# Optimization experiments

Measured on AMD Instinct MI355X. Metric: run time of the kernel, lower is better.

## Reference

```python
import jax, jax.numpy as jnp
import numpy as np

B, C, T, H, W, TS = 4, 512, 2048, 8, 16, 1000
D = C // H  # head_dim = 64
SCALE = D ** -0.5


def _conv1x1(w, b, z):
    # torch Conv1d(dim, dim, 1): (B,C,T) -> (B,C,T)
    return jnp.einsum('oc,bct->bot', w, z) + b[None, :, None]


def _linear(w, b, z):
    # torch Linear: z @ w.T + b, w is (out,in)
    return z @ w.T + b


def _rope(x, cos, sin):
    # x: (B,H,T,D); cos/sin: (T, D//2) broadcast over (B,H)
    x1, x2 = x[..., ::2], x[..., 1::2]
    r = jnp.stack([x1 * cos - x2 * sin, x1 * sin + x2 * cos], axis=-1)
    return r.reshape(x.shape)


def _local(x, cond, qw, qb, kw, kb, vw, vb, ow, ob):
    q = _conv1x1(qw, qb, x)
    k = _conv1x1(kw, kb, cond)
    v = _conv1x1(vw, vb, cond)
    pl = W // 2
    pr = W - pl - 1
    kp = jnp.pad(k, ((0, 0), (0, 0), (pl, pr)))
    vp = jnp.pad(v, ((0, 0), (0, 0), (pl, pr)))
    idx = jnp.arange(T)[:, None] + jnp.arange(W)[None, :]  # (T,W)
    ku = kp[:, :, idx].reshape(B, H, D, T, W)
    vu = vp[:, :, idx].reshape(B, H, D, T, W)
    qh = q.reshape(B, H, D, T)
    dots = jnp.einsum('bhdt,bhdtw->bhtw', qh, ku) * SCALE
    attn = jax.nn.softmax(dots, axis=-1)
    out = jnp.einsum('bhtw,bhdtw->bhdt', attn, vu)
    # faithful to torch: permute(0,1,3,2).contiguous().view(B,C,T)
    out = out.transpose(0, 1, 3, 2).reshape(B, C, T)
    return _conv1x1(ow, ob, out)


def _global(xg, cg, qw, qb, kw, kb, vw, vb, ow, ob):
    # xg, cg: (B,T,C)
    q = _linear(qw, qb, xg).reshape(B, T, H, D).transpose(0, 2, 1, 3)
    k = _linear(kw, kb, cg).reshape(B, T, H, D).transpose(0, 2, 1, 3)
    v = _linear(vw, vb, cg).reshape(B, T, H, D).transpose(0, 2, 1, 3)
    inv_freq = 1.0 / (10000.0 ** (jnp.arange(0, D, 2, dtype=jnp.float32) / D))
    pos = jnp.arange(T, dtype=jnp.float32)
    sinus = pos[:, None] * inv_freq[None, :]  # (T, D//2)
    cos, sin = jnp.cos(sinus), jnp.sin(sinus)
    q = _rope(q, cos, sin)
    k = _rope(k, cos, sin)
    dots = jnp.einsum('bhqd,bhkd->bhqk', q, k) * SCALE
    attn = jax.nn.softmax(dots, axis=-1)
    out = jnp.einsum('bhqk,bhkd->bhqd', attn, v)
    out = out.transpose(0, 2, 1, 3).reshape(B, T, C)
    return _linear(ow, ob, out)


def setup_inputs() -> dict:
    key = jax.random.key(0)
    ks = jax.random.split(key, 20)
    pm = lambda k: jax.random.normal(k, (C, C), dtype=jnp.float32) * 0.02
    pb = lambda k: jax.random.normal(k, (C,), dtype=jnp.float32) * 0.02
    return {
        'x': jax.random.normal(ks[0], (B, C, T), dtype=jnp.float32),
        'cond': jax.random.normal(ks[1], (B, C, T), dtype=jnp.float32),
        't': jax.random.randint(ks[2], (B,), 0, TS),
        'lq_w': pm(ks[3]), 'lq_b': pb(ks[4]),
        'lk_w': pm(ks[5]), 'lk_b': pb(ks[6]),
        'lv_w': pm(ks[7]), 'lv_b': pb(ks[8]),
        'lo_w': pm(ks[9]), 'lo_b': pb(ks[10]),
        'gq_w': pm(ks[11]), 'gq_b': pb(ks[12]),
        'gk_w': pm(ks[13]), 'gk_b': pb(ks[14]),
        'gv_w': pm(ks[15]), 'gv_b': pb(ks[16]),
        'go_w': pm(ks[17]), 'go_b': pb(ks[18]),
    }


def reference(x, cond, t, lq_w, lq_b, lk_w, lk_b, lv_w, lv_b, lo_w, lo_b,
              gq_w, gq_b, gk_w, gk_b, gv_w, gv_b, go_w, go_b):
    ctx_local = _local(x, cond, lq_w, lq_b, lk_w, lk_b, lv_w, lv_b, lo_w, lo_b)
    ctx_global = _global(x.transpose(0, 2, 1), cond.transpose(0, 2, 1),
                         gq_w, gq_b, gk_w, gk_b, gv_w, gv_b, go_w, go_b)
    ctx_global = ctx_global.transpose(0, 2, 1)  # (B,C,T)
    t_norm = t.astype(jnp.float32) / jnp.float32(TS - 1)
    a_g = (1.0 - t_norm)[:, None, None]
    a_l = t_norm[:, None, None]
    return jnp.sqrt(a_g) * ctx_global + jnp.sqrt(a_l) * ctx_local
```

## Files before the change

kernel.cpp:

```cpp
#include <hip/hip_runtime.h>
#include <math.h>

#define BB 4
#define CC 512
#define TT 2048
#define HH 8
#define DD 64

static constexpr float SCALE = 0.125f;
static constexpr float QK_SCALE_LOG2 = 0.125f * 1.4426950408889634f;

typedef __attribute__((ext_vector_type(8)))  short  short8;
typedef __attribute__((ext_vector_type(4)))  float  f32x4;
typedef __attribute__((ext_vector_type(16))) float  f32x16;
typedef __attribute__((ext_vector_type(2)))  unsigned int u32x2;

static __device__ __forceinline__ ushort f2bf(float f) {
    uint u = __float_as_uint(f);
    uint r = (u + 0x7fffu + ((u >> 16) & 1u)) >> 16;
    return (ushort)r;
}
static __device__ __forceinline__ float bf2f(ushort u) {
    return __uint_as_float((uint)u << 16);
}

typedef unsigned int u32;
typedef u32 __attribute__((address_space(1))) gu32;
typedef u32 __attribute__((address_space(3))) lu32;
static __device__ __forceinline__ void gload_lds16(const void* g, void* l) {
    __builtin_amdgcn_global_load_lds((const gu32*)g, (lu32*)l, 16, 0, 0);
}

__global__ __launch_bounds__(256)
void prep_kernel(const float* __restrict__ x, const float* __restrict__ cond,
                 const float* w0, const float* w1, const float* w2, const float* w3,
                 const float* w4, const float* w5, const float* w6, const float* w7,
                 ushort* __restrict__ wbf, ushort* __restrict__ wc,
                 ushort* __restrict__ xtb, ushort* __restrict__ ctb,
                 float* __restrict__ ctab, float* __restrict__ stab)
{
    __shared__ ushort L[64][66];
    int bid = blockIdx.x;
    const int tid = threadIdx.x;

    if (bid < 256) {
        int idx = bid * 256 + tid;
        int i = idx >> 11;
        int t = idx & 2047;
        float ex   = (2.0f * (float)i) / 64.0f;
        float invf = powf(10000.0f, -ex);
        float ang  = (float)t * invf;
        ctab[idx] = cosf(ang);
        stab[idx] = sinf(ang);
        return;
    }
    bid -= 256;
    if (bid < 2048) {
        const float* srcs[8] = {w0, w1, w2, w3, w4, w5, w6, w7};
        int wi = bid >> 8;
        int idx = ((bid & 255) * 256 + tid) * 4;
        float4 v = *(const float4*)&srcs[wi][idx];
        uint lo = (uint)f2bf(v.x) | ((uint)f2bf(v.y) << 16);
        uint hi = (uint)f2bf(v.z) | ((uint)f2bf(v.w) << 16);
        uint2 pk = make_uint2(lo, hi);
        if (wi < 6) {
            *(uint2*)&wbf[(size_t)wi * 262144 + idx] = pk;
        } else {
            int row = idx >> 9, col = idx & 511;
            *(uint2*)&wc[(size_t)row * 1024 + (wi - 6) * 512 + col] = pk;
        }
        return;
    }
    bid -= 2048;
    const int z = bid >> 8;
    const int r = bid & 255;
    const float* in = (z < 4) ? x : cond;
    ushort* outp    = (z < 4) ? xtb : ctb;
    const int b = z & 3;
    const int t0 = (r & 31) * 64, c0 = (r >> 5) * 64;
    const float* inb = in + (size_t)b * CC * TT;
    ushort* outb = outp + (size_t)b * TT * CC;
    const int lc = tid >> 6;
    const int lt = tid & 63;
    #pragma unroll
    for (int i = 0; i < 16; i++) {
        int c = i * 4 + lc;
        L[c][lt] = f2bf(inb[(size_t)(c0 + c) * TT + t0 + lt]);
    }
    __syncthreads();
    #pragma unroll
    for (int i = 0; i < 16; i++) {
        int t = i * 4 + lc;
        outb[(size_t)(t0 + t) * CC + c0 + lt] = L[lt][t];
    }
}

__global__ __launch_bounds__(256)
void transpose_bf16_kernel(const ushort* __restrict__ in, ushort* __restrict__ AG)
{
    __shared__ ushort L[64][66];
    const int t0 = blockIdx.x * 64, c0 = blockIdx.y * 64, b = blockIdx.z;
    const ushort* inb = in + (size_t)b * CC * TT;
    ushort* outb = AG + (size_t)b * TT * 1024;
    const int lc = threadIdx.x >> 6;
    const int lt = threadIdx.x & 63;
    #pragma unroll
    for (int i = 0; i < 16; i++) {
        int c = i * 4 + lc;
        L[c][lt] = inb[(size_t)(c0 + c) * TT + t0 + lt];
    }
    __syncthreads();
    #pragma unroll
    for (int i = 0; i < 16; i++) {
        int t = i * 4 + lc;
        outb[(size_t)(t0 + t) * 1024 + c0 + lt] = L[lt][t];
    }
}

#define GEMM_BODY(Wp, XTp, KD, NB)                                                  \
    __shared__ __align__(16) ushort As[2][128][32];                                 \
    __shared__ __align__(16) ushort Bs[2][NB][32];                                  \
    const int tid  = threadIdx.x;                                                   \
    const int wid  = tid >> 6;                                                      \
    const int lane = tid & 63;                                                      \
    const int x  = lane & 15;                                                       \
    const int gq = lane >> 4;                                                       \
    const int wm = wid >> 1, wn = wid & 1;                                          \
    const int m0 = blockIdx.y * 128;                                                \
    const int n0 = blockIdx.x * NB;                                                 \
    const int srow = lane >> 2;                                                     \
    const int sblk = lane & 3;                                                      \
    f32x4 acc[4][NB / 32];                                                          \
    _Pragma("unroll")                                                               \
    for (int i = 0; i < 4; i++)                                                     \
        _Pragma("unroll")                                                           \
        for (int j = 0; j < NB / 32; j++) acc[i][j] = (f32x4){0.f, 0.f, 0.f, 0.f};  \
    auto stage = [&](int bf, int k0) {                                              \
        _Pragma("unroll")                                                           \
        for (int c = 0; c < 2; c++) {                                               \
            int row = c * 64 + wid * 16 + srow;                                     \
            int dbk = sblk ^ ((row >> 1) & 3);                                      \
            gload_lds16(&Wp[(size_t)(m0 + row) * KD + k0 + dbk * 8],                \
                        &As[bf][c * 64 + wid * 16][0]);                             \
            if (c * 64 < NB)                                                        \
                gload_lds16(&XTp[(size_t)(n0 + row) * KD + k0 + dbk * 8],           \
                            &Bs[bf][c * 64 + wid * 16][0]);                         \
        }                                                                           \
    };                                                                              \
    stage(0, 0);                                                                    \
    __syncthreads();                                                                \
    for (int ks = 0; ks < (KD) / 32; ks++) {                                        \
        int cur = ks & 1;                                                           \
        if (ks < (KD) / 32 - 1) stage(cur ^ 1, (ks + 1) * 32);                      \
        short8 aF[4], bF[NB / 32];                                                  \
        _Pragma("unroll")                                                           \
        for (int mi = 0; mi < 4; mi++) {                                            \
            int row = wm * 64 + mi * 16 + x;                                        \
            aF[mi] = *(const short8*)&As[cur][row][(gq ^ ((row >> 1) & 3)) * 8];    \
        }                                                                           \
        _Pragma("unroll")                                                           \
        for (int nj = 0; nj < NB / 32; nj++) {                                      \
            int row = wn * (NB / 2) + nj * 16 + x;                                  \
            bF[nj] = *(const short8*)&Bs[cur][row][(gq ^ ((row >> 1) & 3)) * 8];    \
        }                                                                           \
        _Pragma("unroll")                                                           \
        for (int mi = 0; mi < 4; mi++)                                              \
            _Pragma("unroll")                                                       \
            for (int nj = 0; nj < NB / 32; nj++)                                    \
                acc[mi][nj] = __builtin_amdgcn_mfma_f32_16x16x32_bf16(aF[mi], bF[nj], acc[mi][nj], 0, 0, 0); \
        __syncthreads();                                                            \
    }

__global__ __launch_bounds__(512, 4)
void gemm6_kernel(const ushort* __restrict__ wbase,
                  const float* __restrict__ b0, const float* __restrict__ b1, const float* __restrict__ b2,
                  const float* __restrict__ b3, const float* __restrict__ b4, const float* __restrict__ b5,
                  const ushort* __restrict__ xtb, const ushort* __restrict__ ctb,
                  ushort* __restrict__ y0, ushort* __restrict__ y1, ushort* __restrict__ y2,
                  ushort* __restrict__ y3, ushort* __restrict__ y4, ushort* __restrict__ y5,
                  const float* __restrict__ ctab, const float* __restrict__ stab)
{
    __shared__ __align__(16) ushort SMEM[16384];
    ushort (*As)[128][32] = (ushort(*)[128][32])&SMEM[0];
    ushort (*Bs)[128][32] = (ushort(*)[128][32])&SMEM[8192];

    const int z = blockIdx.z;
    const ushort* Wp  = wbase + (size_t)z * 262144;
    const float* bias = (z == 0) ? b0 : (z == 1) ? b1 : (z == 2) ? b2 : (z == 3) ? b3 : (z == 4) ? b4 : b5;
    const ushort* XTp = (z == 0 || z == 3) ? xtb : ctb;
    ushort* Y = (z == 0) ? y0 : (z == 1) ? y1 : (z == 2) ? y2 : (z == 3) ? y3 : (z == 4) ? y4 : y5;
    const bool do_rope = (z == 3 || z == 4);
    const bool swp = (z == 5);
    const float qscale = (z == 3) ? QK_SCALE_LOG2 : 1.0f;

    const int tid  = threadIdx.x;
    const int wid  = tid >> 6;
    const int lane = tid & 63;
    const int x  = lane & 15;
    const int gq = lane >> 4;
    const int wm = wid >> 2;
    const int wn = wid & 3;
    const int m0 = blockIdx.y * 128;
    const int n0 = blockIdx.x * 128;
    const int srow = lane >> 2;
    const int sblk = lane & 3;

    f32x4 acc[4][2];
    #pragma unroll
    for (int i = 0; i < 4; i++)
        #pragma unroll
        for (int j = 0; j < 2; j++) acc[i][j] = (f32x4){0.f, 0.f, 0.f, 0.f};

    auto stage = [&](int bf, int k0) {
        int row = wid * 16 + srow;
        int dbk = sblk ^ ((row >> 1) & 3);
        gload_lds16(&Wp[(size_t)(m0 + row) * 512 + k0 + dbk * 8],
                    &As[bf][wid * 16][0]);
        gload_lds16(&XTp[(size_t)(n0 + row) * 512 + k0 + dbk * 8],
                    &Bs[bf][wid * 16][0]);
    };
    stage(0, 0);
    __syncthreads();

    for (int ks = 0; ks < 16; ks++) {
        int cur = ks & 1;
        if (ks < 15) stage(cur ^ 1, (ks + 1) * 32);
        short8 aF[4], bF[2];
        #pragma unroll
        for (int mi = 0; mi < 4; mi++) {
            int row = wm * 64 + mi * 16 + x;
            aF[mi] = *(const short8*)&As[cur][row][(gq ^ ((row >> 1) & 3)) * 8];
        }
        #pragma unroll
        for (int nj = 0; nj < 2; nj++) {
            int row = wn * 32 + nj * 16 + x;
            bF[nj] = *(const short8*)&Bs[cur][row][(gq ^ ((row >> 1) & 3)) * 8];
        }
        if (swp) {
            #pragma unroll
            for (int mi = 0; mi < 4; mi++)
                #pragma unroll
                for (int nj = 0; nj < 2; nj++)
                    acc[mi][nj] = __builtin_amdgcn_mfma_f32_16x16x32_bf16(bF[nj], aF[mi], acc[mi][nj], 0, 0, 0);
        } else {
            #pragma unroll
            for (int mi = 0; mi < 4; mi++)
                #pragma unroll
                for (int nj = 0; nj < 2; nj++)
                    acc[mi][nj] = __builtin_amdgcn_mfma_f32_16x16x32_bf16(aF[mi], bF[nj], acc[mi][nj], 0, 0, 0);
        }
        __syncthreads();
    }

    if (!swp) {
        #pragma unroll
        for (int mi = 0; mi < 4; mi++) {
            const int cL = wm * 64 + mi * 16 + 4 * gq;
            const int mb = m0 + cL;
            float bv[4];
            #pragma unroll
            for (int r = 0; r < 4; r++) bv[r] = bias[mb + r];
            #pragma unroll
            for (int nj = 0; nj < 2; nj++) {
                const int tL = wn * 32 + nj * 16 + x;
                const int tt = (n0 + tL) & 2047;
                f32x4 v = acc[mi][nj];
                v[0] += bv[0]; v[1] += bv[1]; v[2] += bv[2]; v[3] += bv[3];
                if (do_rope) {
                    const int i0 = (mb & 63) >> 1;
                    float c0 = ctab[(size_t)i0 * 2048 + tt],       s0 = stab[(size_t)i0 * 2048 + tt];
                    float c1 = ctab[(size_t)(i0 + 1) * 2048 + tt], s1 = stab[(size_t)(i0 + 1) * 2048 + tt];
                    float e0 = (v[0] * c0 - v[1] * s0) * qscale;
                    float e1 = (v[0] * s0 + v[1] * c0) * qscale;
                    float e2 = (v[2] * c1 - v[3] * s1) * qscale;
                    float e3 = (v[2] * s1 + v[3] * c1) * qscale;
                    v[0] = e0; v[1] = e1; v[2] = e2; v[3] = e3;
                }
                uint lo = (uint)f2bf(v[0]) | ((uint)f2bf(v[1]) << 16);
                uint hi = (uint)f2bf(v[2]) | ((uint)f2bf(v[3]) << 16);
                const int blk = (cL >> 3) ^ (tL & 7);
                *(uint2*)&SMEM[tL * 128 + blk * 8 + (gq & 1) * 4] = make_uint2(lo, hi);
            }
        }
    } else {
        #pragma unroll
        for (int mi = 0; mi < 4; mi++) {
            const int cL = wm * 64 + mi * 16 + x;
            const float bv = bias[m0 + cL];
            #pragma unroll
            for (int nj = 0; nj < 2; nj++) {
                const int tL = wn * 32 + nj * 16 + 4 * gq;
                f32x4 v = acc[mi][nj];
                uint lo = (uint)f2bf(v[0] + bv) | ((uint)f2bf(v[1] + bv) << 16);
                uint hi = (uint)f2bf(v[2] + bv) | ((uint)f2bf(v[3] + bv) << 16);
                const int blk = (tL >> 3) ^ (cL & 7);
                *(uint2*)&SMEM[cL * 128 + blk * 8 + (gq & 1) * 4] = make_uint2(lo, hi);
            }
        }
    }
    __syncthreads();

    if (z <= 3) {
        #pragma unroll
        for (int s = 0; s < 4; s++) {
            const int chunk = s * 512 + tid;
            const int row = chunk >> 4;
            const int blk = chunk & 15;
            uint4 val = *(const uint4*)&SMEM[row * 128 + ((blk ^ (row & 7)) << 3)];
            *(uint4*)&Y[(size_t)(n0 + row) * 512 + m0 + blk * 8] = val;
        }
    } else if (z == 4) {
        const int bidx = n0 >> 11;
        #pragma unroll
        for (int s = 0; s < 4; s++) {
            const int chunk = s * 512 + tid;
            const int row = chunk & 127;
            const int blk = chunk >> 7;
            uint4 val = *(const uint4*)&SMEM[row * 128 + ((blk ^ (row & 7)) << 3)];
            const int tt = (n0 + row) & 2047;
            const int kt = tt >> 6, tk = tt & 63, sb = tk >> 5, qh = tk & 31;
            const int c = m0 + blk * 8;
            const int hh = (c >> 6) & 7, d = c & 63;
            const int kap = d >> 4, hb = (d >> 3) & 1;
            size_t off = (size_t)(bidx * 8 + hh) * 131072
                       + (size_t)(((((kt * 2 + sb) * 4 + kap) * 2 + hb) * 32 + qh) * 8);
            *(uint4*)&Y[off] = val;
        }
    } else {
        const int bidx = n0 >> 11;
        #pragma unroll
        for (int s = 0; s < 4; s++) {
            const int chunk = s * 512 + tid;
            const int rowc = chunk & 127;
            const int blk = chunk >> 7;
            uint4 val = *(const uint4*)&SMEM[rowc * 128 + ((blk ^ (rowc & 7)) << 3)];
            const int c = m0 + rowc;
            const int hh = (c >> 6) & 7, d = c & 63;
            const int qh = d & 31, db = (d >> 5) & 1;
            const int tt0 = (n0 + blk * 8) & 2047;
            const int kt = tt0 >> 6, kk = tt0 & 63;
            const int kc = kk >> 4, hb = (kk >> 3) & 1;
            size_t off = (size_t)(bidx * 8 + hh) * 131072
                       + (size_t)(((((kt * 2 + db) * 4 + kc) * 2 + hb) * 32 + qh) * 8);
            *(uint4*)&Y[off] = val;
        }
    }
}

__global__ __launch_bounds__(256)
void gemm_comb_kernel(const ushort* __restrict__ Wp,
                      const float* __restrict__ bl, const float* __restrict__ bg,
                      const ushort* __restrict__ XTp, float* __restrict__ Y,
                      const int* __restrict__ tarr)
{
    GEMM_BODY(Wp, XTp, 1024, 64)

    const int bidx = (n0 + wn * 32) >> 11;
    float tn = (float)tarr[bidx] / 999.0f;
    float sl = sqrtf(tn), sg = sqrtf(1.0f - tn);

    #pragma unroll
    for (int mi = 0; mi < 4; mi++) {
        const int mb = m0 + wm * 64 + mi * 16 + 4 * gq;
        float bv[4];
        #pragma unroll
        for (int r = 0; r < 4; r++) bv[r] = sl * bl[mb + r] + sg * bg[mb + r];
        #pragma unroll
        for (int nj = 0; nj < 2; nj++) {
            const int tt = (n0 + wn * 32 + nj * 16 + x) & 2047;
            f32x4 v = acc[mi][nj];
            #pragma unroll
            for (int r = 0; r < 4; r++)
                Y[((size_t)bidx * 512 + mb + r) * 2048 + tt] = v[r] + bv[r];
        }
    }
}

__global__ __launch_bounds__(256)
void local_attn_kernel(const ushort* __restrict__ qt, const ushort* __restrict__ kt,
                       const ushort* __restrict__ vt, ushort* __restrict__ outb,
                       const int* __restrict__ tarr)
{
    const int gidx = blockIdx.x * 256 + threadIdx.x;
    const int lane = threadIdx.x & 63;
    const int qu = lane >> 4;
    const int wv = gidx >> 6;
    const int lin = wv * 16 + (lane & 15);
    const int t = lin & (TT - 1);
    const int h = (lin >> 11) & (HH - 1);
    const int b = lin >> 14;
    const size_t rb = (size_t)b * TT;
    const int co = h * DD + qu * 16;
    const float wl = sqrtf((float)tarr[b] / 999.0f);

    float qf[16];
    {
        const ushort* qp = qt + (rb + t) * 512 + co;
        #pragma unroll
        for (int i = 0; i < 2; i++) {
            short8 v = *(const short8*)&qp[i * 8];
            #pragma unroll
            for (int j = 0; j < 8; j++) qf[i * 8 + j] = bf2f((ushort)v[j]);
        }
    }

    int koff[16]; float msk[16];
    #pragma unroll
    for (int w = 0; w < 16; w++) {
        int kidx = t + w - 8;
        msk[w]  = (kidx >= 0 && kidx < TT) ? 1.0f : 0.0f;
        koff[w] = min(max(kidx, 0), TT - 1);
    }

    float dots[16];
    #pragma unroll
    for (int w = 0; w < 16; w++) {
        const ushort* kp = kt + (rb + koff[w]) * 512 + co;
        float d0 = 0.f, d1 = 0.f;
        #pragma unroll
        for (int i = 0; i < 2; i++) {
            short8 v = *(const short8*)&kp[i * 8];
            #pragma unroll
            for (int j = 0; j < 8; j += 2) {
                d0 = fmaf(qf[i * 8 + j],     bf2f((ushort)v[j]),     d0);
                d1 = fmaf(qf[i * 8 + j + 1], bf2f((ushort)v[j + 1]), d1);
            }
        }
        dots[w] = d0 + d1;
    }
    #pragma unroll
    for (int w = 0; w < 16; w++) {
        dots[w] += __shfl_xor(dots[w], 16);
        dots[w] += __shfl_xor(dots[w], 32);
    }

    float m = -1e30f;
    #pragma unroll
    for (int w = 0; w < 16; w++) { dots[w] = dots[w] * SCALE * msk[w]; m = fmaxf(m, dots[w]); }
    float p[16], s = 0.f;
    #pragma unroll
    for (int w = 0; w < 16; w++) { p[w] = __expf(dots[w] - m); s += p[w]; }
    float inv = wl / s;
    #pragma unroll
    for (int w = 0; w < 16; w++) p[w] *= msk[w] * inv;

    float oa[16];
    #pragma unroll
    for (int d = 0; d < 16; d++) oa[d] = 0.f;
    #pragma unroll
    for (int w = 0; w < 16; w++) {
        const ushort* vp = vt + (rb + koff[w]) * 512 + co;
        #pragma unroll
        for (int i = 0; i < 2; i++) {
            short8 v = *(const short8*)&vp[i * 8];
            #pragma unroll
            for (int j = 0; j < 8; j++)
                oa[i * 8 + j] = fmaf(p[w], bf2f((ushort)v[j]), oa[i * 8 + j]);
        }
    }

    ushort* op = outb + ((size_t)b * CC + h * DD + (t >> 5)) * TT + (size_t)(t & 31) * DD + qu * 16;
    #pragma unroll
    for (int i = 0; i < 2; i++) {
        uint w0 = (uint)f2bf(oa[i * 8 + 0]) | ((uint)f2bf(oa[i * 8 + 1]) << 16);
        uint w1 = (uint)f2bf(oa[i * 8 + 2]) | ((uint)f2bf(oa[i * 8 + 3]) << 16);
        uint w2 = (uint)f2bf(oa[i * 8 + 4]) | ((uint)f2bf(oa[i * 8 + 5]) << 16);
        uint w3 = (uint)f2bf(oa[i * 8 + 6]) | ((uint)f2bf(oa[i * 8 + 7]) << 16);
        *(uint4*)&op[i * 8] = make_uint4(w0, w1, w2, w3);
    }
}

__global__ __launch_bounds__(512)
void flash_global_kernel(const ushort* __restrict__ qtd, const ushort* __restrict__ KT,
                         const ushort* __restrict__ VT, ushort* __restrict__ AG,
                         const int* __restrict__ tarr)
{
    __shared__ __align__(16) ushort Ks[2][2][4096];
    __shared__ __align__(16) ushort Vs[2][2][4096];

    const int tid  = threadIdx.x;
    const int grp  = tid >> 8;
    const int t8   = tid & 255;
    const int w    = t8 >> 6;
    const int lane = tid & 63;
    const int qh   = lane & 31;
    const int h    = lane >> 5;

    const int bid = blockIdx.x;
    const int sw  = (bid & 7) * 64 + (bid >> 3);
    const int qt  = sw & 15;
    const int p   = sw >> 4;
    const int hh  = p & 7, b = p >> 3;

    const size_t kvbase = (size_t)p * 131072 + (size_t)grp * (16 * 4096);
    const size_t btd    = (size_t)b * TT;
    const int q_glob = qt * 128 + w * 32 + qh;
    const float sg_mix = sqrtf(1.0f - (float)tarr[b] / 999.0f);

    short8 aQ[4];
    {
        const ushort* qrow = qtd + (btd + q_glob) * 512 + hh * 64;
        #pragma unroll
        for (int kap = 0; kap < 4; kap++)
            aQ[kap] = *(const short8*)&qrow[kap * 16 + h * 8];
    }

    f32x16 oacc[2];
    #pragma unroll
    for (int d = 0; d < 2; d++)
        #pragma unroll
        for (int r = 0; r < 16; r++) oacc[d][r] = 0.f;
    float l_run = 0.0f;

    const ushort* kA = KT + kvbase + (size_t)(2 * w) * 512 + lane * 8;
    const ushort* vA = VT + kvbase + (size_t)(2 * w) * 512 + lane * 8;

    auto issue = [&](int buf, int kt) {
        const size_t off = (size_t)kt * 4096;
        gload_lds16(kA + off,       &Ks[grp][buf][(2 * w) * 512]);
        gload_lds16(kA + off + 512, &Ks[grp][buf][(2 * w + 1) * 512]);
        gload_lds16(vA + off,       &Vs[grp][buf][(2 * w) * 512]);
        gload_lds16(vA + off + 512, &Vs[grp][buf][(2 * w + 1) * 512]);
    };
    issue(0, 0);

    int cur = 0;
    for (int kt = 0; kt < 16; kt++) {
        __syncthreads();
        if (kt < 15) issue(cur ^ 1, kt + 1);

        const ushort* KsC = &Ks[grp][cur][0];
        const ushort* VsC = &Vs[grp][cur][0];

        f32x16 ST[2];
        #pragma unroll
        for (int sb = 0; sb < 2; sb++)
            #pragma unroll
            for (int r = 0; r < 16; r++) ST[sb][r] = 0.f;
        __builtin_amdgcn_s_setprio(1);
        #pragma unroll
        for (int sb = 0; sb < 2; sb++)
            #pragma unroll
            for (int kap = 0; kap < 4; kap++) {
                short8 aK = *(const short8*)&KsC[(sb * 4 + kap) * 512 + lane * 8];
                ST[sb] = __builtin_amdgcn_mfma_f32_32x32x16_bf16(aK, aQ[kap], ST[sb], 0, 0, 0);
            }
        __builtin_amdgcn_s_setprio(0);

        float s0 = 0.f, s1 = 0.f, s2 = 0.f, s3 = 0.f;
        #pragma unroll
        for (int sb = 0; sb < 2; sb++)
            #pragma unroll
            for (int r = 0; r < 16; r += 4) {
                ST[sb][r + 0] = __builtin_amdgcn_exp2f(ST[sb][r + 0]);
                ST[sb][r + 1] = __builtin_amdgcn_exp2f(ST[sb][r + 1]);
                ST[sb][r + 2] = __builtin_amdgcn_exp2f(ST[sb][r + 2]);
                ST[sb][r + 3] = __builtin_amdgcn_exp2f(ST[sb][r + 3]);
                s0 += ST[sb][r + 0]; s1 += ST[sb][r + 1];
                s2 += ST[sb][r + 2]; s3 += ST[sb][r + 3];
            }
        l_run += (s0 + s1) + (s2 + s3);

        short8 bP[4];
        #pragma unroll
        for (int sb = 0; sb < 2; sb++)
            #pragma unroll
            for (int kcp = 0; kcp < 2; kcp++) {
                const int rb2 = kcp * 8;
                uint ca, cb, cc, cd;
                asm("v_cvt_pk_bf16_f32 %0, %1, %2" : "=v"(ca) : "v"(ST[sb][rb2 + 0]), "v"(ST[sb][rb2 + 1]));
                asm("v_cvt_pk_bf16_f32 %0, %1, %2" : "=v"(cb) : "v"(ST[sb][rb2 + 2]), "v"(ST[sb][rb2 + 3]));
                asm("v_cvt_pk_bf16_f32 %0, %1, %2" : "=v"(cc) : "v"(ST[sb][rb2 + 4]), "v"(ST[sb][rb2 + 5]));
                asm("v_cvt_pk_bf16_f32 %0, %1, %2" : "=v"(cd) : "v"(ST[sb][rb2 + 6]), "v"(ST[sb][rb2 + 7]));
                u32x2 r1 = __builtin_amdgcn_permlane32_swap(ca, cc, false, false);
                u32x2 r2 = __builtin_amdgcn_permlane32_swap(cb, cd, false, false);
                uint4 bu = make_uint4(r1[0], r2[0], r1[1], r2[1]);
                bP[sb * 2 + kcp] = __builtin_bit_cast(short8, bu);
            }

        __builtin_amdgcn_s_setprio(1);
        #pragma unroll
        for (int db = 0; db < 2; db++)
            #pragma unroll
            for (int kc = 0; kc < 4; kc++) {
                short8 aV = *(const short8*)&VsC[(db * 4 + kc) * 512 + lane * 8];
                oacc[db] = __builtin_amdgcn_mfma_f32_32x32x16_bf16(aV, bP[kc], oacc[db], 0, 0, 0);
            }
        __builtin_amdgcn_s_setprio(0);
        cur ^= 1;
    }

    __syncthreads();
    f32x4* OP = (f32x4*)&Ks[0][0][0];
    float* LP = (float*)&Vs[0][0][0];
    if (grp == 1) {
        #pragma unroll
        for (int j = 0; j < 8; j++)
            OP[j * 256 + t8] = (f32x4){oacc[j >> 2][(j & 3) * 4 + 0], oacc[j >> 2][(j & 3) * 4 + 1],
                                       oacc[j >> 2][(j & 3) * 4 + 2], oacc[j >> 2][(j & 3) * 4 + 3]};
        LP[t8] = l_run;
    }
    __syncthreads();
    if (grp == 0) {
        #pragma unroll
        for (int j = 0; j < 8; j++) {
            f32x4 o = OP[j * 256 + t8];
            oacc[j >> 2][(j & 3) * 4 + 0] += o[0];
            oacc[j >> 2][(j & 3) * 4 + 1] += o[1];
            oacc[j >> 2][(j & 3) * 4 + 2] += o[2];
            oacc[j >> 2][(j & 3) * 4 + 3] += o[3];
        }
        l_run += LP[t8];
        float ltot = l_run + __shfl_xor(l_run, 32);
        float inv = sg_mix / ltot;
        ushort* agrow = AG + (btd + q_glob) * 1024 + 512 + hh * 64;
        #pragma unroll
        for (int db = 0; db < 2; db++)
            #pragma unroll
            for (int rq = 0; rq < 4; rq++) {
                const int d0 = db * 32 + rq * 8 + h * 4;
                uint lo = (uint)f2bf(oacc[db][rq * 4 + 0] * inv) | ((uint)f2bf(oacc[db][rq * 4 + 1] * inv) << 16);
                uint hi = (uint)f2bf(oacc[db][rq * 4 + 2] * inv) | ((uint)f2bf(oacc[db][rq * 4 + 3] * inv) << 16);
                *(uint2*)&agrow[d0] = make_uint2(lo, hi);
            }
    }
}

extern "C" void kernel_launch(void* const* d_in, const int* in_sizes, int n_in,
                              void* d_out, int out_size, void* d_ws, size_t ws_size,
                              hipStream_t stream)
{
    const float* x    = (const float*)d_in[0];
    const float* cond = (const float*)d_in[1];
    const int*   tarr = (const int*)d_in[2];
    const float* lq_w = (const float*)d_in[3];
    const float* lq_b = (const float*)d_in[4];
    const float* lk_w = (const float*)d_in[5];
    const float* lk_b = (const float*)d_in[6];
    const float* lv_w = (const float*)d_in[7];
    const float* lv_b = (const float*)d_in[8];
    const float* lo_w = (const float*)d_in[9];
    const float* lo_b = (const float*)d_in[10];
    const float* gq_w = (const float*)d_in[11];
    const float* gq_b = (const float*)d_in[12];
    const float* gk_w = (const float*)d_in[13];
    const float* gk_b = (const float*)d_in[14];
    const float* gv_w = (const float*)d_in[15];
    const float* gv_b = (const float*)d_in[16];
    const float* go_w = (const float*)d_in[17];
    const float* go_b = (const float*)d_in[18];
    float* out = (float*)d_out;

    const size_t N = (size_t)BB * CC * TT;
    char* w = (char*)d_ws;
    ushort* xtb = (ushort*)w; w += N * 2;
    ushort* ctb = (ushort*)w; w += N * 2;
    ushort* lq  = (ushort*)w; w += N * 2;
    ushort* lk  = (ushort*)w; w += N * 2;
    ushort* lv  = (ushort*)w; w += N * 2;
    ushort* gqb = (ushort*)w; w += N * 2;
    ushort* ktb = (ushort*)w; w += N * 2;
    ushort* vtb = (ushort*)w; w += N * 2;
    ushort* scr = (ushort*)w; w += N * 2;
    ushort* AG  = (ushort*)w; w += (size_t)BB * TT * 1024 * 2;
    ushort* wbf = (ushort*)w; w += (size_t)6 * 512 * 512 * 2;
    ushort* wc  = (ushort*)w; w += (size_t)512 * 1024 * 2;
    float* ctab = (float*)w;  w += (size_t)32 * 2048 * 4;
    float* stab = (float*)w;

    dim3 blk(256);

    prep_kernel<<<dim3(4352), blk, 0, stream>>>(x, cond,
                                                lq_w, lk_w, lv_w, gq_w, gk_w, gv_w, lo_w, go_w,
                                                wbf, wc, xtb, ctb, ctab, stab);

    gemm6_kernel<<<dim3(64, 4, 6), dim3(512), 0, stream>>>(wbf, lq_b, lk_b, lv_b, gq_b, gk_b, gv_b,
                                                           xtb, ctb, lq, lk, lv, gqb, ktb, vtb, ctab, stab);

    local_attn_kernel<<<dim3(BB * HH * TT * 4 / 256), blk, 0, stream>>>(lq, lk, lv, scr, tarr);
    transpose_bf16_kernel<<<dim3(32, 8, BB), blk, 0, stream>>>(scr, AG);

    flash_global_kernel<<<dim3(512), dim3(512), 0, stream>>>(gqb, ktb, vtb, AG, tarr);

    gemm_comb_kernel<<<dim3(128, 4), blk, 0, stream>>>(wc, lo_b, go_b, AG, out, tarr);
}
```

Measured before the change: 154.9 us.

## Fuse local and global attention into one interleaved-block kernel launch

```diff
diff --git a/kernel.cpp b/kernel.cpp
--- a/kernel.cpp
+++ b/kernel.cpp
@@ -376,253 +376,255 @@
     }
 }
 
-__global__ __launch_bounds__(256)
-void local_attn_kernel(const ushort* __restrict__ qt, const ushort* __restrict__ kt,
+__global__ __launch_bounds__(512)
+void fused_attn_kernel(const ushort* __restrict__ qtd, const ushort* __restrict__ KT,
+                       const ushort* __restrict__ VT, ushort* __restrict__ AG,
+                       const ushort* __restrict__ qt, const ushort* __restrict__ kt,
                        const ushort* __restrict__ vt, ushort* __restrict__ outb,
                        const int* __restrict__ tarr)
 {
-    const int gidx = blockIdx.x * 256 + threadIdx.x;
-    const int lane = threadIdx.x & 63;
-    const int qu = lane >> 4;
-    const int wv = gidx >> 6;
-    const int lin = wv * 16 + (lane & 15);
-    const int t = lin & (TT - 1);
-    const int h = (lin >> 11) & (HH - 1);
-    const int b = lin >> 14;
-    const size_t rb = (size_t)b * TT;
-    const int co = h * DD + qu * 16;
-    const float wl = sqrtf((float)tarr[b] / 999.0f);
-
-    float qf[16];
-    {
-        const ushort* qp = qt + (rb + t) * 512 + co;
-        #pragma unroll
-        for (int i = 0; i < 2; i++) {
-            short8 v = *(const short8*)&qp[i * 8];
-            #pragma unroll
-            for (int j = 0; j < 8; j++) qf[i * 8 + j] = bf2f((ushort)v[j]);
-        }
-    }
-
-    int koff[16]; float msk[16];
-    #pragma unroll
-    for (int w = 0; w < 16; w++) {
-        int kidx = t + w - 8;
-        msk[w]  = (kidx >= 0 && kidx < TT) ? 1.0f : 0.0f;
-        koff[w] = min(max(kidx, 0), TT - 1);
-    }
-
-    float dots[16];
-    #pragma unroll
-    for (int w = 0; w < 16; w++) {
-        const ushort* kp = kt + (rb + koff[w]) * 512 + co;
-        float d0 = 0.f, d1 = 0.f;
-        #pragma unroll
-        for (int i = 0; i < 2; i++) {
-            short8 v = *(const short8*)&kp[i * 8];
-            #pragma unroll
-            for (int j = 0; j < 8; j += 2) {
-                d0 = fmaf(qf[i * 8 + j],     bf2f((ushort)v[j]),     d0);
-                d1 = fmaf(qf[i * 8 + j + 1], bf2f((ushort)v[j + 1]), d1);
-            }
-        }
-        dots[w] = d0 + d1;
-    }
-    #pragma unroll
-    for (int w = 0; w < 16; w++) {
-        dots[w] += __shfl_xor(dots[w], 16);
-        dots[w] += __shfl_xor(dots[w], 32);
-    }
-
-    float m = -1e30f;
-    #pragma unroll
-    for (int w = 0; w < 16; w++) { dots[w] = dots[w] * SCALE * msk[w]; m = fmaxf(m, dots[w]); }
-    float p[16], s = 0.f;
-    #pragma unroll
-    for (int w = 0; w < 16; w++) { p[w] = __expf(dots[w] - m); s += p[w]; }
-    float inv = wl / s;
-    #pragma unroll
-    for (int w = 0; w < 16; w++) p[w] *= msk[w] * inv;
-
-    float oa[16];
-    #pragma unroll
-    for (int d = 0; d < 16; d++) oa[d] = 0.f;
-    #pragma unroll
-    for (int w = 0; w < 16; w++) {
-        const ushort* vp = vt + (rb + koff[w]) * 512 + co;
-        #pragma unroll
-        for (int i = 0; i < 2; i++) {
-            short8 v = *(const short8*)&vp[i * 8];
-            #pragma unroll
-            for (int j = 0; j < 8; j++)
-                oa[i * 8 + j] = fmaf(p[w], bf2f((ushort)v[j]), oa[i * 8 + j]);
-        }
-    }
-
-    ushort* op = outb + ((size_t)b * CC + h * DD + (t >> 5)) * TT + (size_t)(t & 31) * DD + qu * 16;
-    #pragma unroll
-    for (int i = 0; i < 2; i++) {
-        uint w0 = (uint)f2bf(oa[i * 8 + 0]) | ((uint)f2bf(oa[i * 8 + 1]) << 16);
-        uint w1 = (uint)f2bf(oa[i * 8 + 2]) | ((uint)f2bf(oa[i * 8 + 3]) << 16);
-        uint w2 = (uint)f2bf(oa[i * 8 + 4]) | ((uint)f2bf(oa[i * 8 + 5]) << 16);
-        uint w3 = (uint)f2bf(oa[i * 8 + 6]) | ((uint)f2bf(oa[i * 8 + 7]) << 16);
-        *(uint4*)&op[i * 8] = make_uint4(w0, w1, w2, w3);
-    }
-}
-
-__global__ __launch_bounds__(512)
-void flash_global_kernel(const ushort* __restrict__ qtd, const ushort* __restrict__ KT,
-                         const ushort* __restrict__ VT, ushort* __restrict__ AG,
-                         const int* __restrict__ tarr)
-{
     __shared__ __align__(16) ushort Ks[2][2][4096];
     __shared__ __align__(16) ushort Vs[2][2][4096];
 
-    const int tid  = threadIdx.x;
-    const int grp  = tid >> 8;
-    const int t8   = tid & 255;
-    const int w    = t8 >> 6;
-    const int lane = tid & 63;
-    const int qh   = lane & 31;
-    const int h    = lane >> 5;
-
-    const int bid = blockIdx.x;
-    const int sw  = (bid & 7) * 64 + (bid >> 3);
-    const int qt  = sw & 15;
-    const int p   = sw >> 4;
-    const int hh  = p & 7, b = p >> 3;
-
-    const size_t kvbase = (size_t)p * 131072 + (size_t)grp * (16 * 4096);
-    const size_t btd    = (size_t)b * TT;
-    const int q_glob = qt * 128 + w * 32 + qh;
-    const float sg_mix = sqrtf(1.0f - (float)tarr[b] / 999.0f);
-
-    short8 aQ[4];
-    {
-        const ushort* qrow = qtd + (btd + q_glob) * 512 + hh * 64;
-        #pragma unroll
-        for (int kap = 0; kap < 4; kap++)
-            aQ[kap] = *(const short8*)&qrow[kap * 16 + h * 8];
-    }
-
-    f32x16 oacc[2];
-    #pragma unroll
-    for (int d = 0; d < 2; d++)
-        #pragma unroll
-        for (int r = 0; r < 16; r++) oacc[d][r] = 0.f;
-    float l_run = 0.0f;
-
-    const ushort* kA = KT + kvbase + (size_t)(2 * w) * 512 + lane * 8;
-    const ushort* vA = VT + kvbase + (size_t)(2 * w) * 512 + lane * 8;
-
-    auto issue = [&](int buf, int kt) {
-        const size_t off = (size_t)kt * 4096;
-        gload_lds16(kA + off,       &Ks[grp][buf][(2 * w) * 512]);
-        gload_lds16(kA + off + 512, &Ks[grp][buf][(2 * w + 1) * 512]);
-        gload_lds16(vA + off,       &Vs[grp][buf][(2 * w) * 512]);
-        gload_lds16(vA + off + 512, &Vs[grp][buf][(2 * w + 1) * 512]);
-    };
-    issue(0, 0);
-
-    int cur = 0;
-    for (int kt = 0; kt < 16; kt++) {
+    const int chunk = blockIdx.x >> 3;
+    const int sub   = blockIdx.x & 7;
+
+    if ((chunk & 1) == 0) {
+        const int fbid = (chunk >> 1) * 8 + sub;
+        const int tid  = threadIdx.x;
+        const int grp  = tid >> 8;
+        const int t8   = tid & 255;
+        const int w    = t8 >> 6;
+        const int lane = tid & 63;
+        const int qh   = lane & 31;
+        const int h    = lane >> 5;
+
+        const int sw  = (fbid & 7) * 64 + (fbid >> 3);
+        const int qt2 = sw & 15;
+        const int p   = sw >> 4;
+        const int hh  = p & 7, b = p >> 3;
+
+        const size_t kvbase = (size_t)p * 131072 + (size_t)grp * (16 * 4096);
+        const size_t btd    = (size_t)b * TT;
+        const int q_glob = qt2 * 128 + w * 32 + qh;
+        const float sg_mix = sqrtf(1.0f - (float)tarr[b] / 999.0f);
+
+        short8 aQ[4];
+        {
+            const ushort* qrow = qtd + (btd + q_glob) * 512 + hh * 64;
+            #pragma unroll
+            for (int kap = 0; kap < 4; kap++)
+                aQ[kap] = *(const short8*)&qrow[kap * 16 + h * 8];
+        }
+
+        f32x16 oacc[2];
+        #pragma unroll
+        for (int d = 0; d < 2; d++)
+            #pragma unroll
+            for (int r = 0; r < 16; r++) oacc[d][r] = 0.f;
+        float l_run = 0.0f;
+
+        const ushort* kA = KT + kvbase + (size_t)(2 * w) * 512 + lane * 8;
+        const ushort* vA = VT + kvbase + (size_t)(2 * w) * 512 + lane * 8;
+
+        auto issue = [&](int buf, int kti) {
+            const size_t off = (size_t)kti * 4096;
+            gload_lds16(kA + off,       &Ks[grp][buf][(2 * w) * 512]);
+            gload_lds16(kA + off + 512, &Ks[grp][buf][(2 * w + 1) * 512]);
+            gload_lds16(vA + off,       &Vs[grp][buf][(2 * w) * 512]);
+            gload_lds16(vA + off + 512, &Vs[grp][buf][(2 * w + 1) * 512]);
+        };
+        issue(0, 0);
+
+        int cur = 0;
+        for (int kti = 0; kti < 16; kti++) {
+            __syncthreads();
+            if (kti < 15) issue(cur ^ 1, kti + 1);
+
+            const ushort* KsC = &Ks[grp][cur][0];
+            const ushort* VsC = &Vs[grp][cur][0];
+
+            f32x16 ST[2];
+            #pragma unroll
+            for (int sb = 0; sb < 2; sb++)
+                #pragma unroll
+                for (int r = 0; r < 16; r++) ST[sb][r] = 0.f;
+            __builtin_amdgcn_s_setprio(1);
+            #pragma unroll
+            for (int sb = 0; sb < 2; sb++)
+                #pragma unroll
+                for (int kap = 0; kap < 4; kap++) {
+                    short8 aK = *(const short8*)&KsC[(sb * 4 + kap) * 512 + lane * 8];
+                    ST[sb] = __builtin_amdgcn_mfma_f32_32x32x16_bf16(aK, aQ[kap], ST[sb], 0, 0, 0);
+                }
+            __builtin_amdgcn_s_setprio(0);
+
+            float s0 = 0.f, s1 = 0.f, s2 = 0.f, s3 = 0.f;
+            #pragma unroll
+            for (int sb = 0; sb < 2; sb++)
+                #pragma unroll
+                for (int r = 0; r < 16; r += 4) {
+                    ST[sb][r + 0] = __builtin_amdgcn_exp2f(ST[sb][r + 0]);
+                    ST[sb][r + 1] = __builtin_amdgcn_exp2f(ST[sb][r + 1]);
+                    ST[sb][r + 2] = __builtin_amdgcn_exp2f(ST[sb][r + 2]);
+                    ST[sb][r + 3] = __builtin_amdgcn_exp2f(ST[sb][r + 3]);
+                    s0 += ST[sb][r + 0]; s1 += ST[sb][r + 1];
+                    s2 += ST[sb][r + 2]; s3 += ST[sb][r + 3];
+                }
+            l_run += (s0 + s1) + (s2 + s3);
+
+            short8 bP[4];
+            #pragma unroll
+            for (int sb = 0; sb < 2; sb++)
+                #pragma unroll
+                for (int kcp = 0; kcp < 2; kcp++) {
+                    const int rb2 = kcp * 8;
+                    uint ca, cb, cc, cd;
+                    asm("v_cvt_pk_bf16_f32 %0, %1, %2" : "=v"(ca) : "v"(ST[sb][rb2 + 0]), "v"(ST[sb][rb2 + 1]));
+                    asm("v_cvt_pk_bf16_f32 %0, %1, %2" : "=v"(cb) : "v"(ST[sb][rb2 + 2]), "v"(ST[sb][rb2 + 3]));
+                    asm("v_cvt_pk_bf16_f32 %0, %1, %2" : "=v"(cc) : "v"(ST[sb][rb2 + 4]), "v"(ST[sb][rb2 + 5]));
+                    asm("v_cvt_pk_bf16_f32 %0, %1, %2" : "=v"(cd) : "v"(ST[sb][rb2 + 6]), "v"(ST[sb][rb2 + 7]));
+                    u32x2 r1 = __builtin_amdgcn_permlane32_swap(ca, cc, false, false);
+                    u32x2 r2 = __builtin_amdgcn_permlane32_swap(cb, cd, false, false);
+                    uint4 bu = make_uint4(r1[0], r2[0], r1[1], r2[1]);
+                    bP[sb * 2 + kcp] = __builtin_bit_cast(short8, bu);
+                }
+
+            __builtin_amdgcn_s_setprio(1);
+            #pragma unroll
+            for (int db = 0; db < 2; db++)
+                #pragma unroll
+                for (int kc = 0; kc < 4; kc++) {
+                    short8 aV = *(const short8*)&VsC[(db * 4 + kc) * 512 + lane * 8];
+                    oacc[db] = __builtin_amdgcn_mfma_f32_32x32x16_bf16(aV, bP[kc], oacc[db], 0, 0, 0);
+                }
+            __builtin_amdgcn_s_setprio(0);
+            cur ^= 1;
+        }
+
         __syncthreads();
-        if (kt < 15) issue(cur ^ 1, kt + 1);
-
-        const ushort* KsC = &Ks[grp][cur][0];
-        const ushort* VsC = &Vs[grp][cur][0];
-
-        f32x16 ST[2];
-        #pragma unroll
-        for (int sb = 0; sb < 2; sb++)
-            #pragma unroll
-            for (int r = 0; r < 16; r++) ST[sb][r] = 0.f;
-        __builtin_amdgcn_s_setprio(1);
-        #pragma unroll
-        for (int sb = 0; sb < 2; sb++)
-            #pragma unroll
-            for (int kap = 0; kap < 4; kap++) {
-                short8 aK = *(const short8*)&KsC[(sb * 4 + kap) * 512 + lane * 8];
-                ST[sb] = __builtin_amdgcn_mfma_f32_32x32x16_bf16(aK, aQ[kap], ST[sb], 0, 0, 0);
+        f32x4* OP = (f32x4*)&Ks[0][0][0];
+        float* LP = (float*)&Vs[0][0][0];
+        if (grp == 1) {
+            #pragma unroll
+            for (int j = 0; j < 8; j++)
+                OP[j * 256 + t8] = (f32x4){oacc[j >> 2][(j & 3) * 4 + 0], oacc[j >> 2][(j & 3) * 4 + 1],
+                                           oacc[j >> 2][(j & 3) * 4 + 2], oacc[j >> 2][(j & 3) * 4 + 3]};
+            LP[t8] = l_run;
+        }
+        __syncthreads();
+        if (grp == 0) {
+            #pragma unroll
+            for (int j = 0; j < 8; j++) {
+                f32x4 o = OP[j * 256 + t8];
+                oacc[j >> 2][(j & 3) * 4 + 0] += o[0];
+                oacc[j >> 2][(j & 3) * 4 + 1] += o[1];
+                oacc[j >> 2][(j & 3) * 4 + 2] += o[2];
+                oacc[j >> 2][(j & 3) * 4 + 3] += o[3];
             }
-        __builtin_amdgcn_s_setprio(0);
-
-        float s0 = 0.f, s1 = 0.f, s2 = 0.f, s3 = 0.f;
-        #pragma unroll
-        for (int sb = 0; sb < 2; sb++)
-            #pragma unroll
-            for (int r = 0; r < 16; r += 4) {
-                ST[sb][r + 0] = __builtin_amdgcn_exp2f(ST[sb][r + 0]);
-                ST[sb][r + 1] = __builtin_amdgcn_exp2f(ST[sb][r + 1]);
-                ST[sb][r + 2] = __builtin_amdgcn_exp2f(ST[sb][r + 2]);
-                ST[sb][r + 3] = __builtin_amdgcn_exp2f(ST[sb][r + 3]);
-                s0 += ST[sb][r + 0]; s1 += ST[sb][r + 1];
-                s2 += ST[sb][r + 2]; s3 += ST[sb][r + 3];
+            l_run += LP[t8];
+            float ltot = l_run + __shfl_xor(l_run, 32);
+            float inv = sg_mix / ltot;
+            ushort* agrow = AG + (btd + q_glob) * 1024 + 512 + hh * 64;
+            #pragma unroll
+            for (int db = 0; db < 2; db++)
+                #pragma unroll
+                for (int rq = 0; rq < 4; rq++) {
+                    const int d0 = db * 32 + rq * 8 + h * 4;
+                    uint lo = (uint)f2bf(oacc[db][rq * 4 + 0] * inv) | ((uint)f2bf(oacc[db][rq * 4 + 1] * inv) << 16);
+                    uint hi = (uint)f2bf(oacc[db][rq * 4 + 2] * inv) | ((uint)f2bf(oacc[db][rq * 4 + 3] * inv) << 16);
+                    *(uint2*)&agrow[d0] = make_uint2(lo, hi);
+                }
+        }
+    } else {
+        const int lbid = (chunk >> 1) * 8 + sub;
+        const int gidx = lbid * 512 + threadIdx.x;
+        const int lane = threadIdx.x & 63;
+        const int qu = lane >> 4;
+        const int wv = gidx >> 6;
+        const int lin = wv * 16 + (lane & 15);
+        const int t = lin & (TT - 1);
+        const int h = (lin >> 11) & (HH - 1);
+        const int b = lin >> 14;
+        const size_t rb = (size_t)b * TT;
+        const int co = h * DD + qu * 16;
+        const float wl = sqrtf((float)tarr[b] / 999.0f);
+
+        float qf[16];
+        {
+            const ushort* qp = qt + (rb + t) * 512 + co;
+            #pragma unroll
+            for (int i = 0; i < 2; i++) {
+                short8 v = *(const short8*)&qp[i * 8];
+                #pragma unroll
+                for (int j = 0; j < 8; j++) qf[i * 8 + j] = bf2f((ushort)v[j]);
             }
-        l_run += (s0 + s1) + (s2 + s3);
-
-        short8 bP[4];
-        #pragma unroll
-        for (int sb = 0; sb < 2; sb++)
-            #pragma unroll
-            for (int kcp = 0; kcp < 2; kcp++) {
-                const int rb2 = kcp * 8;
-                uint ca, cb, cc, cd;
-                asm("v_cvt_pk_bf16_f32 %0, %1, %2" : "=v"(ca) : "v"(ST[sb][rb2 + 0]), "v"(ST[sb][rb2 + 1]));
-                asm("v_cvt_pk_bf16_f32 %0, %1, %2" : "=v"(cb) : "v"(ST[sb][rb2 + 2]), "v"(ST[sb][rb2 + 3]));
-                asm("v_cvt_pk_bf16_f32 %0, %1, %2" : "=v"(cc) : "v"(ST[sb][rb2 + 4]), "v"(ST[sb][rb2 + 5]));
-                asm("v_cvt_pk_bf16_f32 %0, %1, %2" : "=v"(cd) : "v"(ST[sb][rb2 + 6]), "v"(ST[sb][rb2 + 7]));
-                u32x2 r1 = __builtin_amdgcn_permlane32_swap(ca, cc, false, false);
-                u32x2 r2 = __builtin_amdgcn_permlane32_swap(cb, cd, false, false);
-                uint4 bu = make_uint4(r1[0], r2[0], r1[1], r2[1]);
-                bP[sb * 2 + kcp] = __builtin_bit_cast(short8, bu);
+        }
+
+        int koff[16]; float msk[16];
+        #pragma unroll
+        for (int w = 0; w < 16; w++) {
+            int kidx = t + w - 8;
+            msk[w]  = (kidx >= 0 && kidx < TT) ? 1.0f : 0.0f;
+            koff[w] = min(max(kidx, 0), TT - 1);
+        }
+
+        float dots[16];
+        #pragma unroll
+        for (int w = 0; w < 16; w++) {
+            const ushort* kp = kt + (rb + koff[w]) * 512 + co;
+            float d0 = 0.f, d1 = 0.f;
+            #pragma unroll
+            for (int i = 0; i < 2; i++) {
+                short8 v = *(const short8*)&kp[i * 8];
+                #pragma unroll
+                for (int j = 0; j < 8; j += 2) {
+                    d0 = fmaf(qf[i * 8 + j],     bf2f((ushort)v[j]),     d0);
+                    d1 = fmaf(qf[i * 8 + j + 1], bf2f((ushort)v[j + 1]), d1);
+                }
             }
-
-        __builtin_amdgcn_s_setprio(1);
-        #pragma unroll
-        for (int db = 0; db < 2; db++)
-            #pragma unroll
-            for (int kc = 0; kc < 4; kc++) {
-                short8 aV = *(const short8*)&VsC[(db * 4 + kc) * 512 + lane * 8];
-                oacc[db] = __builtin_amdgcn_mfma_f32_32x32x16_bf16(aV, bP[kc], oacc[db], 0, 0, 0);
+            dots[w] = d0 + d1;
+        }
+        #pragma unroll
+        for (int w = 0; w < 16; w++) {
+            dots[w] += __shfl_xor(dots[w], 16);
+            dots[w] += __shfl_xor(dots[w], 32);
+        }
+
+        float m = -1e30f;
+        #pragma unroll
+        for (int w = 0; w < 16; w++) { dots[w] = dots[w] * SCALE * msk[w]; m = fmaxf(m, dots[w]); }
+        float p[16], s = 0.f;
+        #pragma unroll
+        for (int w = 0; w < 16; w++) { p[w] = __expf(dots[w] - m); s += p[w]; }
+        float inv = wl / s;
+        #pragma unroll
+        for (int w = 0; w < 16; w++) p[w] *= msk[w] * inv;
+
+        float oa[16];
+        #pragma unroll
+        for (int d = 0; d < 16; d++) oa[d] = 0.f;
+        #pragma unroll
+        for (int w = 0; w < 16; w++) {
+            const ushort* vp = vt + (rb + koff[w]) * 512 + co;
+            #pragma unroll
+            for (int i = 0; i < 2; i++) {
+                short8 v = *(const short8*)&vp[i * 8];
+                #pragma unroll
+                for (int j = 0; j < 8; j++)
+                    oa[i * 8 + j] = fmaf(p[w], bf2f((ushort)v[j]), oa[i * 8 + j]);
             }
-        __builtin_amdgcn_s_setprio(0);
-        cur ^= 1;
-    }
-
-    __syncthreads();
-    f32x4* OP = (f32x4*)&Ks[0][0][0];
-    float* LP = (float*)&Vs[0][0][0];
-    if (grp == 1) {
-        #pragma unroll
-        for (int j = 0; j < 8; j++)
-            OP[j * 256 + t8] = (f32x4){oacc[j >> 2][(j & 3) * 4 + 0], oacc[j >> 2][(j & 3) * 4 + 1],
-                                       oacc[j >> 2][(j & 3) * 4 + 2], oacc[j >> 2][(j & 3) * 4 + 3]};
-        LP[t8] = l_run;
-    }
-    __syncthreads();
-    if (grp == 0) {
-        #pragma unroll
-        for (int j = 0; j < 8; j++) {
-            f32x4 o = OP[j * 256 + t8];
-            oacc[j >> 2][(j & 3) * 4 + 0] += o[0];
-            oacc[j >> 2][(j & 3) * 4 + 1] += o[1];
-            oacc[j >> 2][(j & 3) * 4 + 2] += o[2];
-            oacc[j >> 2][(j & 3) * 4 + 3] += o[3];
-        }
-        l_run += LP[t8];
-        float ltot = l_run + __shfl_xor(l_run, 32);
-        float inv = sg_mix / ltot;
-        ushort* agrow = AG + (btd + q_glob) * 1024 + 512 + hh * 64;
-        #pragma unroll
-        for (int db = 0; db < 2; db++)
-            #pragma unroll
-            for (int rq = 0; rq < 4; rq++) {
-                const int d0 = db * 32 + rq * 8 + h * 4;
-                uint lo = (uint)f2bf(oacc[db][rq * 4 + 0] * inv) | ((uint)f2bf(oacc[db][rq * 4 + 1] * inv) << 16);
-                uint hi = (uint)f2bf(oacc[db][rq * 4 + 2] * inv) | ((uint)f2bf(oacc[db][rq * 4 + 3] * inv) << 16);
-                *(uint2*)&agrow[d0] = make_uint2(lo, hi);
-            }
+        }
+
+        ushort* op = outb + ((size_t)b * CC + h * DD + (t >> 5)) * TT + (size_t)(t & 31) * DD + qu * 16;
+        #pragma unroll
+        for (int i = 0; i < 2; i++) {
+            uint w0 = (uint)f2bf(oa[i * 8 + 0]) | ((uint)f2bf(oa[i * 8 + 1]) << 16);
+            uint w1 = (uint)f2bf(oa[i * 8 + 2]) | ((uint)f2bf(oa[i * 8 + 3]) << 16);
+            uint w2 = (uint)f2bf(oa[i * 8 + 4]) | ((uint)f2bf(oa[i * 8 + 5]) << 16);
+            uint w3 = (uint)f2bf(oa[i * 8 + 6]) | ((uint)f2bf(oa[i * 8 + 7]) << 16);
+            *(uint4*)&op[i * 8] = make_uint4(w0, w1, w2, w3);
+        }
     }
 }
 
@@ -677,10 +679,10 @@
     gemm6_kernel<<<dim3(64, 4, 6), dim3(512), 0, stream>>>(wbf, lq_b, lk_b, lv_b, gq_b, gk_b, gv_b,
                                                            xtb, ctb, lq, lk, lv, gqb, ktb, vtb, ctab, stab);
 
-    local_attn_kernel<<<dim3(BB * HH * TT * 4 / 256), blk, 0, stream>>>(lq, lk, lv, scr, tarr);
+    fused_attn_kernel<<<dim3(1024), dim3(512), 0, stream>>>(gqb, ktb, vtb, AG,
+                                                            lq, lk, lv, scr, tarr);
+
     transpose_bf16_kernel<<<dim3(32, 8, BB), blk, 0, stream>>>(scr, AG);
 
-    flash_global_kernel<<<dim3(512), dim3(512), 0, stream>>>(gqb, ktb, vtb, AG, tarr);
-
     gemm_comb_kernel<<<dim3(128, 4), blk, 0, stream>>>(wc, lo_b, go_b, AG, out, tarr);
 }
```

After: 177.4 us. 1.15x slower.
